# Performance work log

Hardware: AMD Instinct MI355X
Metric: run time of the kernel (lower is better)

## Reference

```python
import jax, jax.numpy as jnp
import numpy as np

N = 4096
DEG = 16.0
KC = 64  # max closed-neighborhood size supported (deg~16 graph => safe)


def setup_inputs() -> dict:
    key = jax.random.key(0)
    ks = jax.random.split(key, 6)
    u = jax.random.uniform(ks[0], (N, N))
    upper = jnp.triu((u < (DEG / N)).astype(jnp.float32), k=1)
    adj = upper + upper.T  # symmetric 0/1, zero diagonal
    d = 64
    return {
        'adj': adj,
        'e_w': jax.random.normal(ks[1], (15, d), dtype=jnp.float32) * 0.25,
        'e_b': jnp.zeros((d,), jnp.float32),
        'w1': jax.random.normal(ks[2], (3, d, d), dtype=jnp.float32) * 0.125,
        'b1': jnp.zeros((3, d), jnp.float32),
        'w2': jax.random.normal(ks[3], (3, d, d), dtype=jnp.float32) * 0.125,
        'b2': jnp.zeros((3, d), jnp.float32),
        'eps': jnp.zeros((3,), jnp.float32),
    }


def cr_feat(adj):
    n = adj.shape[0]
    m = adj + jnp.eye(n, dtype=adj.dtype)  # closed-neighborhood indicator rows [N,N]
    k = m.sum(1)                            # |S_v|
    D = m @ adj                             # D[v,u] = degree of u inside S_v (A symmetric)
    E = 0.5 * jnp.sum(m * D, axis=1)        # edges inside S_v
    W = jnp.sum(m * D * (D - 1.0) * 0.5, axis=1)  # wedges inside S_v
    vals, idx = jax.lax.top_k(m, KC)        # members of S_v (padded)
    valid = (vals > 0.5).astype(adj.dtype)
    sub = adj[idx[:, :, None], idx[:, None, :]]        # [N,KC,KC] induced subgraph
    sub = sub * valid[:, :, None] * valid[:, None, :]
    T = jnp.einsum('vij,vjk,vki->v', sub, sub, sub) / 6.0  # triangles inside S_v
    f3 = T
    f2 = W - 3.0 * T
    f1 = E * (k - 2.0) - 2.0 * f2 - 3.0 * f3
    tot = k * (k - 1.0) * (k - 2.0) / 6.0   # C(k,3) = total triples
    f0 = tot - f1 - f2 - f3
    f = jnp.stack([f0, f1, f2, f3], axis=1)
    f = jnp.where((k >= 3.0)[:, None], f, 0.0)  # original skips |nb|<3
    return f / (jnp.sum(f, axis=1, keepdims=True) + 1e-10)


def ww_feat(adj):
    a2 = adj @ adj
    a4 = a2 @ a2                             # matrix_power(adj, 4)
    vals, _ = jax.lax.top_k(a4, 8)           # per-row sort desc, top 8
    return vals


def degree_feat(adj):
    d = adj.sum(1)
    diag_a2 = jnp.einsum('vu,uv->v', adj, adj)  # diag(A@A)
    return jnp.stack([d, d ** 2, diag_a2], axis=1)


def _forward(adj, e_w, e_b, w1, b1, w2, b2, eps):
    feats = jnp.concatenate([cr_feat(adj), ww_feat(adj), degree_feat(adj)], axis=1)  # [N,15]
    x = feats @ e_w + e_b
    for i in range(3):
        h = (1.0 + eps[i]) * x + adj @ x
        x = jax.nn.relu(h @ w1[i] + b1[i]) @ w2[i] + b2[i]
    return x.sum(0)


def reference(adj, e_w, e_b, w1, b1, w2, b2, eps):
    return _forward(adj, e_w, e_b, w1, b1, w2, b2, eps)
```

## Files before the change

kernel.cpp:

```cpp
#include <hip/hip_runtime.h>
#include <hip/hip_bf16.h>
#include <stdint.h>

#define NN 4096
#define MAXNZ 1536


__global__ __launch_bounds__(256) void scan_k(const float* __restrict__ adj,
                                              int* __restrict__ nbr,
                                              int* __restrict__ deg,
                                              unsigned long long* __restrict__ abits,
                                              float* __restrict__ feats) {
    __shared__ int nlist[4][64];
    int tid = threadIdx.x;
    int wv = tid >> 6, ln = tid & 63;
    int v = blockIdx.x * 4 + wv;
    size_t rb = (size_t)v * NN;
    int total = 0;
    unsigned long long w0 = 0;
    for (int base = 0; base < NN; base += 256) {
        float v0 = adj[rb + base + ln];
        float v1 = adj[rb + base + 64 + ln];
        float v2 = adj[rb + base + 128 + ln];
        float v3 = adj[rb + base + 192 + ln];
        int q4 = (base >> 8) << 2;
        {
            unsigned long long m = __ballot(v0 > 0.5f);
            if (v0 > 0.5f) {
                int pos = total + __popcll(m & ((1ull << ln) - 1ull));
                if (pos < 64) nlist[wv][pos] = base + ln;
            }
            if (ln == q4 + 0) w0 = m;
            total += __popcll(m);
        }
        {
            unsigned long long m = __ballot(v1 > 0.5f);
            if (v1 > 0.5f) {
                int pos = total + __popcll(m & ((1ull << ln) - 1ull));
                if (pos < 64) nlist[wv][pos] = base + 64 + ln;
            }
            if (ln == q4 + 1) w0 = m;
            total += __popcll(m);
        }
        {
            unsigned long long m = __ballot(v2 > 0.5f);
            if (v2 > 0.5f) {
                int pos = total + __popcll(m & ((1ull << ln) - 1ull));
                if (pos < 64) nlist[wv][pos] = base + 128 + ln;
            }
            if (ln == q4 + 2) w0 = m;
            total += __popcll(m);
        }
        {
            unsigned long long m = __ballot(v3 > 0.5f);
            if (v3 > 0.5f) {
                int pos = total + __popcll(m & ((1ull << ln) - 1ull));
                if (pos < 64) nlist[wv][pos] = base + 192 + ln;
            }
            if (ln == q4 + 3) w0 = m;
            total += __popcll(m);
        }
    }
    abits[(size_t)v * 64 + ln] = w0;
    int degL = min(total, 64);
    if (ln < degL) nbr[v * 64 + ln] = nlist[wv][ln];
    if (ln == 0) {
        deg[v] = total;
        float degf = (float)total;
        feats[v * 16 + 12] = degf;
        feats[v * 16 + 13] = degf * degf;
        feats[v * 16 + 14] = degf;
    }
}

__global__ __launch_bounds__(256) void cra2_k(const unsigned long long* __restrict__ abits,
                                              const int* __restrict__ nbr,
                                              const int* __restrict__ deg,
                                              unsigned int* __restrict__ csr,
                                              int* __restrict__ cnt,
                                              unsigned char* __restrict__ ncb,
                                              float* __restrict__ feats) {
    __shared__ __align__(16) unsigned int smem[NN + 136];
    int tid = threadIdx.x;
    int bid = blockIdx.x;
    int wv = tid >> 6, ln = tid & 63;

    if (bid < NN) {
        unsigned int* acc   = smem;
        int* us             = (int*)(smem + NN);
        int* dus            = (int*)(smem + NN + 64);
        unsigned int* wsumS = smem + NN + 128;
        int v = bid;
        {
            uint4 z = {0u, 0u, 0u, 0u};
            #pragma unroll
            for (int i = 0; i < 4; i++) ((uint4*)acc)[tid + 256 * i] = z;
        }
        int dv = min(deg[v], 64);
        if (tid < dv) {
            int u = nbr[v * 64 + tid];
            us[tid] = u;
            dus[tid] = min(deg[u], 64);
        }
        __syncthreads();
        for (int p = tid; p < dv * 64; p += 256) {
            int i = p >> 6, wi = p & 63;
            int u = us[i];
            if (wi < dus[i]) atomicAdd(&acc[nbr[u * 64 + wi]], 1u);
        }
        __syncthreads();
        unsigned int local = 0;
        #pragma unroll
        for (int m = 0; m < 16; m++) {
            unsigned int a = acc[tid + 256 * m];
            local += (a + 14u) / 15u;
        }
        unsigned int incl = local;
        #pragma unroll
        for (int off = 1; off < 64; off <<= 1) {
            unsigned int n = (unsigned int)__shfl_up((int)incl, off, 64);
            if (ln >= off) incl += n;
        }
        if (ln == 63) wsumS[wv] = incl;
        __syncthreads();
        unsigned int wprefix = 0, tot = 0;
        #pragma unroll
        for (int q = 0; q < 4; q++) {
            unsigned int s = wsumS[q];
            if (q < wv) wprefix += s;
            tot += s;
        }
        unsigned int pos = wprefix + (incl - local);
        unsigned short* dst = (unsigned short*)((char*)csr + (size_t)v * 3072);
        #pragma unroll
        for (int m = 0; m < 16; m++) {
            unsigned int a = acc[tid + 256 * m];
            unsigned int col = (unsigned int)(tid + 256 * m);
            while (a) {
                unsigned int w = a > 15u ? 15u : a;
                if (pos < 1520u) dst[pos] = (unsigned short)((w << 12) | col);
                pos++;
                a -= w;
            }
        }
        unsigned int bs = min(tot, 1520u);
        unsigned int padto = (bs + 7u) & ~7u;
        if (tid < padto - bs) dst[bs + tid] = (unsigned short)(bs + tid);
        if (tid == 0) {
            cnt[v] = (int)bs;
            ncb[v] = (unsigned char)(padto >> 3);
        }
    } else {
        unsigned long long* rows = (unsigned long long*)smem;
        int* mems = (int*)(smem + 1024);
        int v = (bid - NN) * 4 + wv;

        int dv = deg[v];
        int degL = min(dv, 64);
        int c = min(dv + 1, 64);

        int nl = (ln < degL) ? nbr[v * 64 + ln] : 0;
        int isless = (ln < degL && nl < v) ? 1 : 0;
        int pos = isless;
        #pragma unroll
        for (int off = 32; off; off >>= 1) pos += __shfl_xor(pos, off, 64);

        int mem = 0;
        if (ln < c) {
            if (ln < pos)       mem = nl;
            else if (ln == pos) mem = v;
            else                mem = nbr[v * 64 + ln - 1];
        }
        mems[wv * 64 + ln] = mem;
        __syncthreads();

        unsigned long long mask = 0ull;
        {
            const unsigned long long* rowb = abits + (size_t)mem * 64;
            for (int j = 0; j < c; j++) {
                int mj = mems[wv * 64 + j];
                unsigned long long w = rowb[mj >> 6];
                mask |= ((w >> (mj & 63)) & 1ull) << j;
            }
        }
        if (ln >= c) mask = 0ull;
        rows[wv * 64 + ln] = mask;
        __syncthreads();

        int tpart = 0;
        float epart = 0.f, wpart = 0.f;
        if (ln < c) {
            unsigned long long mm = mask;
            while (mm) {
                int j = __ffsll(mm) - 1;
                mm &= mm - 1;
                tpart += __popcll(mask & rows[wv * 64 + j]);
            }
            if (ln != pos) {
                int cn = __popcll(rows[wv * 64 + pos] & mask);
                float D = (float)cn + 1.0f;
                epart = D;
                wpart = D * (D - 1.0f) * 0.5f;
            }
        }
        float es = epart, wsum2 = wpart;
        int ts = tpart;
        #pragma unroll
        for (int off = 32; off; off >>= 1) {
            es += __shfl_xor(es, off, 64);
            wsum2 += __shfl_xor(wsum2, off, 64);
            ts += __shfl_xor(ts, off, 64);
        }

        if (ln == 0) {
            float degf = (float)dv;
            float k = degf + 1.0f;
            float E = 0.5f * (es + degf);
            float W = wsum2 + degf * (degf - 1.0f) * 0.5f;
            float T = (float)ts / 6.0f;
            float f3 = T;
            float f2 = W - 3.0f * T;
            float f1 = E * (k - 2.0f) - 2.0f * f2 - 3.0f * f3;
            float tot2 = k * (k - 1.0f) * (k - 2.0f) / 6.0f;
            float f0 = tot2 - f1 - f2 - f3;
            if (k < 3.0f) { f0 = f1 = f2 = f3 = 0.f; }
            float s = f0 + f1 + f2 + f3 + 1e-10f;
            feats[v * 16 + 0] = f0 / s;
            feats[v * 16 + 1] = f1 / s;
            feats[v * 16 + 2] = f2 / s;
            feats[v * 16 + 3] = f3 / s;
        }
    }
}

__global__ __launch_bounds__(1024) void order_k(const unsigned char* __restrict__ ncb,
                                                int* __restrict__ ord) {
    __shared__ unsigned int bcnt[192];
    __shared__ unsigned int bbase[192];
    int tid = threadIdx.x;
    if (tid < 192) bcnt[tid] = 0u;
    __syncthreads();
    unsigned char myk[4];
    #pragma unroll
    for (int j = 0; j < 4; j++) {
        int v = tid * 4 + j;
        myk[j] = ncb[v];
        atomicAdd(&bcnt[myk[j]], 1u);
    }
    __syncthreads();
    if (tid == 0) {
        unsigned int run = 0;
        for (int b = 191; b >= 0; b--) { bbase[b] = run; run += bcnt[b]; }
    }
    __syncthreads();
    #pragma unroll
    for (int j = 0; j < 4; j++) {
        int v = tid * 4 + j;
        unsigned int p = atomicAdd(&bbase[myk[j]], 1u);
        ord[p] = v;
    }
}

__device__ __forceinline__ void do8(unsigned int* acc, uint4 E, unsigned int W) {
    atomicAdd(&acc[E.x & 0xFFFu],         W * ((E.x >> 12) & 0xFu));
    atomicAdd(&acc[(E.x >> 16) & 0xFFFu], W * (E.x >> 28));
    atomicAdd(&acc[E.y & 0xFFFu],         W * ((E.y >> 12) & 0xFu));
    atomicAdd(&acc[(E.y >> 16) & 0xFFFu], W * (E.y >> 28));
    atomicAdd(&acc[E.z & 0xFFFu],         W * ((E.z >> 12) & 0xFu));
    atomicAdd(&acc[(E.z >> 16) & 0xFFFu], W * (E.z >> 28));
    atomicAdd(&acc[E.w & 0xFFFu],         W * ((E.w >> 12) & 0xFu));
    atomicAdd(&acc[(E.w >> 16) & 0xFFFu], W * (E.w >> 28));
}

__global__ __launch_bounds__(512) void a4row_k(const unsigned int* __restrict__ csr,
                                               const int* __restrict__ cnt,
                                               const unsigned char* __restrict__ ncb,
                                               const int* __restrict__ ord,
                                               const float* __restrict__ feats,
                                               const float* __restrict__ e_w,
                                               const float* __restrict__ e_b,
                                               float* __restrict__ x0) {
    __shared__ unsigned int acc[NN];
    __shared__ __align__(16) unsigned int rowe[MAXNZ];
    __shared__ unsigned int wtops[64];
    int tid = threadIdx.x;
    int wv = tid >> 6, ln = tid & 63;
    int v = ord[blockIdx.x];

    {
        uint4 z = {0u, 0u, 0u, 0u};
        #pragma unroll
        for (int i = 0; i < 2; i++) ((uint4*)acc)[tid + 512 * i] = z;
    }

    int nv = cnt[v];
    int nvp = (nv + 7) & ~7;
    const unsigned short* rowv = (const unsigned short*)((const char*)csr + (size_t)v * 3072);
    for (int i = tid; i < nvp; i += 512) {
        unsigned int e = rowv[i];
        unsigned int u = e & 0xFFFu;
        unsigned int w = e >> 12;
        unsigned int nc = w ? (unsigned int)ncb[u] : 0u;
        rowe[i] = u | (w << 12) | (nc << 16);
    }
    __syncthreads();

    const uint4* csr4 = (const uint4*)csr;
    for (int i0 = wv * 4; i0 < nvp; i0 += 32) {
        uint4 q = *(const uint4*)&rowe[i0];
        int c1 = (int)(q.x >> 16);
        int c2 = c1 + (int)(q.y >> 16);
        int c3 = c2 + (int)(q.z >> 16);
        int tot = c3 + (int)(q.w >> 16);
        unsigned int s0 = ((q.x & 0xFFFu) * 192u + 1024u)                    | (((q.x >> 12) & 0xFu) << 21);
        unsigned int s1 = ((q.y & 0xFFFu) * 192u + 1024u - (unsigned int)c1) | (((q.y >> 12) & 0xFu) << 21);
        unsigned int s2 = ((q.z & 0xFFFu) * 192u + 1024u - (unsigned int)c2) | (((q.z >> 12) & 0xFu) << 21);
        unsigned int s3 = ((q.w & 0xFFFu) * 192u + 1024u - (unsigned int)c3) | (((q.w >> 12) & 0xFu) << 21);
        for (int g = ln; g < tot; g += 64) {
            unsigned int sel = (g < c1) ? s0 : ((g < c2) ? s1 : ((g < c3) ? s2 : s3));
            unsigned int idx = (sel & 0x1FFFFFu) + (unsigned int)g - 1024u;
            uint4 E = csr4[idx];
            do8(acc, E, sel >> 21);
        }
    }
    __syncthreads();

    unsigned int best[8];
    #pragma unroll
    for (int q = 0; q < 8; q++) best[q] = 0u;
    #pragma unroll
    for (int m = 0; m < 8; m++) {
        unsigned int val = acc[tid + 512 * m];
        if (val > best[7]) {
            best[7] = val;
            #pragma unroll
            for (int s = 7; s > 0; s--) {
                if (best[s] > best[s - 1]) {
                    unsigned int t2 = best[s - 1]; best[s - 1] = best[s]; best[s] = t2;
                } else break;
            }
        }
    }

    unsigned int wave_val = 0u;
    #pragma unroll
    for (int r = 0; r < 8; r++) {
        unsigned int m = best[0];
        #pragma unroll
        for (int off = 32; off; off >>= 1)
            m = max(m, (unsigned int)__shfl_xor((int)m, off, 64));
        unsigned long long bb = __ballot(best[0] == m);
        int src = __ffsll(bb) - 1;
        if (ln == src) {
            #pragma unroll
            for (int s = 0; s < 7; s++) best[s] = best[s + 1];
            best[7] = 0u;
        }
        if (ln == r) wave_val = m;
    }
    if (ln < 8) wtops[wv * 8 + ln] = wave_val;
    __syncthreads();

    if (wv == 0) {
        unsigned int cand = wtops[ln];
        unsigned int myv = 0u;
        #pragma unroll
        for (int r = 0; r < 8; r++) {
            unsigned int m = cand;
            #pragma unroll
            for (int off = 32; off; off >>= 1)
                m = max(m, (unsigned int)__shfl_xor((int)m, off, 64));
            unsigned long long bb = __ballot(cand == m);
            int src = __ffsll(bb) - 1;
            if (ln == src) cand = 0u;
            if (ln == r) myv = m;
        }
        int d = ln;
        float s = e_b[d];
        s += feats[v * 16 + 0]  * e_w[0 * 64 + d];
        s += feats[v * 16 + 1]  * e_w[1 * 64 + d];
        s += feats[v * 16 + 2]  * e_w[2 * 64 + d];
        s += feats[v * 16 + 3]  * e_w[3 * 64 + d];
        #pragma unroll
        for (int j = 0; j < 8; j++) {
            float mj = (float)(unsigned int)__shfl((int)myv, j, 64);
            s += mj * e_w[(4 + j) * 64 + d];
        }
        s += feats[v * 16 + 12] * e_w[12 * 64 + d];
        s += feats[v * 16 + 13] * e_w[13 * 64 + d];
        s += feats[v * 16 + 14] * e_w[14 * 64 + d];
        x0[(size_t)v * 64 + d] = s;
    }
}

__global__ __launch_bounds__(256) void layer_k(const float* __restrict__ xin,
                                               float* __restrict__ xout,
                                               const float* __restrict__ w1,
                                               const float* __restrict__ b1,
                                               const float* __restrict__ w2,
                                               const float* __restrict__ b2,
                                               const float* __restrict__ eps,
                                               const int* __restrict__ nbr,
                                               const int* __restrict__ deg,
                                               float* __restrict__ out,
                                               int li) {
    __shared__ float wL[4096];
    __shared__ float h[4][64], t[4][64];
    int tid = threadIdx.x;
    int wv = tid >> 6, d = tid & 63;
    int v = blockIdx.x * 4 + wv;

    {
        const float4* src = (const float4*)(w1 + li * 4096);
        #pragma unroll
        for (int i = 0; i < 4; i++) ((float4*)wL)[tid + 256 * i] = src[tid + 256 * i];
    }

    float xv = xin[(size_t)v * 64 + d];
    int dv = min(deg[v], 64);
    const int* nl = nbr + v * 64;
    float agg = 0.f;
    int j = 0;
    for (; j + 4 <= dv; j += 4) {
        int n0 = nl[j], n1 = nl[j + 1], n2 = nl[j + 2], n3 = nl[j + 3];
        float a0 = xin[(size_t)n0 * 64 + d];
        float a1 = xin[(size_t)n1 * 64 + d];
        float a2v = xin[(size_t)n2 * 64 + d];
        float a3 = xin[(size_t)n3 * 64 + d];
        agg += (a0 + a1) + (a2v + a3);
    }
    for (; j < dv; j++) agg += xin[(size_t)nl[j] * 64 + d];
    float hv = (1.0f + eps[li]) * xv + agg;
    h[wv][d] = hv;
    __syncthreads();

    float s = b1[li * 64 + d];
    #pragma unroll 8
    for (int k = 0; k < 64; k++) s += h[wv][k] * wL[k * 64 + d];
    s = fmaxf(s, 0.f);
    t[wv][d] = s;
    __syncthreads();

    {
        const float4* src = (const float4*)(w2 + li * 4096);
        #pragma unroll
        for (int i = 0; i < 4; i++) ((float4*)wL)[tid + 256 * i] = src[tid + 256 * i];
    }
    __syncthreads();

    float o = b2[li * 64 + d];
    #pragma unroll 8
    for (int k = 0; k < 64; k++) o += t[wv][k] * wL[k * 64 + d];
    if (li == 2) {
        h[wv][d] = o;
        __syncthreads();
        if (wv == 0)
            atomicAdd(&out[d], (h[0][d] + h[1][d]) + (h[2][d] + h[3][d]));
    } else {
        xout[(size_t)v * 64 + d] = o;
    }
}

extern "C" void kernel_launch(void* const* d_in, const int* in_sizes, int n_in,
                              void* d_out, int out_size, void* d_ws, size_t ws_size,
                              hipStream_t stream) {
    const float* adj = (const float*)d_in[0];
    const float* e_w = (const float*)d_in[1];
    const float* e_b = (const float*)d_in[2];
    const float* w1  = (const float*)d_in[3];
    const float* b1  = (const float*)d_in[4];
    const float* w2  = (const float*)d_in[5];
    const float* b2  = (const float*)d_in[6];
    const float* eps = (const float*)d_in[7];
    float* out = (float*)d_out;

    char* ws = (char*)d_ws;
    unsigned int*       csr     = (unsigned int*)(ws);
    int*                nbr     = (int*)(ws + 25165824);
    int*                deg     = (int*)(ws + 26214400);
    int*                cnt     = (int*)(ws + 26230784);
    float*              feats   = (float*)(ws + 26247168);
    float*              x0      = (float*)(ws + 26509312);
    float*              x1      = (float*)(ws + 27557888);
    unsigned long long* abits   = (unsigned long long*)(ws + 28868608);
    unsigned char*      ncb     = (unsigned char*)(ws + 30965760);
    int*                ord     = (int*)(ws + 30969856);

    hipMemsetAsync(out, 0, 64 * sizeof(float), stream);
    scan_k<<<1024, 256, 0, stream>>>(adj, nbr, deg, abits, feats);
    cra2_k<<<5120, 256, 0, stream>>>(abits, nbr, deg, csr, cnt, ncb, feats);
    order_k<<<1, 1024, 0, stream>>>(ncb, ord);
    a4row_k<<<4096, 512, 0, stream>>>(csr, cnt, ncb, ord, feats, e_w, e_b, x0);
    layer_k<<<1024, 256, 0, stream>>>(x0, x1, w1, b1, w2, b2, eps, nbr, deg, out, 0);
    layer_k<<<1024, 256, 0, stream>>>(x1, x0, w1, b1, w2, b2, eps, nbr, deg, out, 1);
    layer_k<<<1024, 256, 0, stream>>>(x0, x1, w1, b1, w2, b2, eps, nbr, deg, out, 2);
}
```

Baseline: 278.1 us.

## Vectorize adjacency scan with float4 and interleave CSR storage layout

```diff
diff --git a/kernel.cpp b/kernel.cpp
--- a/kernel.cpp
+++ b/kernel.cpp
@@ -18,46 +18,19 @@
     size_t rb = (size_t)v * NN;
     int total = 0;
     unsigned long long w0 = 0;
+    const float4* row4 = (const float4*)(adj + rb);
     for (int base = 0; base < NN; base += 256) {
-        float v0 = adj[rb + base + ln];
-        float v1 = adj[rb + base + 64 + ln];
-        float v2 = adj[rb + base + 128 + ln];
-        float v3 = adj[rb + base + 192 + ln];
+        float4 f = row4[(base >> 2) + ln];
         int q4 = (base >> 8) << 2;
-        {
-            unsigned long long m = __ballot(v0 > 0.5f);
-            if (v0 > 0.5f) {
+        #pragma unroll
+        for (int j = 0; j < 4; j++) {
+            float vj = (j == 0) ? f.x : (j == 1) ? f.y : (j == 2) ? f.z : f.w;
+            unsigned long long m = __ballot(vj > 0.5f);
+            if (vj > 0.5f) {
                 int pos = total + __popcll(m & ((1ull << ln) - 1ull));
-                if (pos < 64) nlist[wv][pos] = base + ln;
-            }
-            if (ln == q4 + 0) w0 = m;
-            total += __popcll(m);
-        }
-        {
-            unsigned long long m = __ballot(v1 > 0.5f);
-            if (v1 > 0.5f) {
-                int pos = total + __popcll(m & ((1ull << ln) - 1ull));
-                if (pos < 64) nlist[wv][pos] = base + 64 + ln;
-            }
-            if (ln == q4 + 1) w0 = m;
-            total += __popcll(m);
-        }
-        {
-            unsigned long long m = __ballot(v2 > 0.5f);
-            if (v2 > 0.5f) {
-                int pos = total + __popcll(m & ((1ull << ln) - 1ull));
-                if (pos < 64) nlist[wv][pos] = base + 128 + ln;
-            }
-            if (ln == q4 + 2) w0 = m;
-            total += __popcll(m);
-        }
-        {
-            unsigned long long m = __ballot(v3 > 0.5f);
-            if (v3 > 0.5f) {
-                int pos = total + __popcll(m & ((1ull << ln) - 1ull));
-                if (pos < 64) nlist[wv][pos] = base + 192 + ln;
-            }
-            if (ln == q4 + 3) w0 = m;
+                if (pos < 64) nlist[wv][pos] = base + 4 * ln + j;
+            }
+            if (ln == q4 + j) w0 = m;
             total += __popcll(m);
         }
     }
@@ -131,6 +104,10 @@
             tot += s;
         }
         unsigned int pos = wprefix + (incl - local);
+        unsigned int bs = min(tot, 1520u);
+        unsigned int padto = (bs + 7u) & ~7u;
+        unsigned int D = padto >> 3;
+        unsigned long long M = (unsigned long long)(0xFFFFFFFFu / max(D, 1u)) + 1ull;
         unsigned short* dst = (unsigned short*)((char*)csr + (size_t)v * 3072);
         #pragma unroll
         for (int m = 0; m < 16; m++) {
@@ -138,14 +115,21 @@
             unsigned int col = (unsigned int)(tid + 256 * m);
             while (a) {
                 unsigned int w = a > 15u ? 15u : a;
-                if (pos < 1520u) dst[pos] = (unsigned short)((w << 12) | col);
+                if (pos < 1520u) {
+                    unsigned int q = (unsigned int)(((unsigned long long)pos * M) >> 32);
+                    unsigned int r = pos - q * D;
+                    dst[8u * r + q] = (unsigned short)((w << 12) | col);
+                }
                 pos++;
                 a -= w;
             }
         }
-        unsigned int bs = min(tot, 1520u);
-        unsigned int padto = (bs + 7u) & ~7u;
-        if (tid < padto - bs) dst[bs + tid] = (unsigned short)(bs + tid);
+        if (tid < padto - bs) {
+            unsigned int p = bs + tid;
+            unsigned int q = (unsigned int)(((unsigned long long)p * M) >> 32);
+            unsigned int r = p - q * D;
+            dst[8u * r + q] = (unsigned short)(p & 0xFFFu);
+        }
         if (tid == 0) {
             cnt[v] = (int)bs;
             ncb[v] = (unsigned char)(padto >> 3);
@@ -179,8 +163,8 @@
             const unsigned long long* rowb = abits + (size_t)mem * 64;
             for (int j = 0; j < c; j++) {
                 int mj = mems[wv * 64 + j];
-                unsigned long long w = rowb[mj >> 6];
-                mask |= ((w >> (mj & 63)) & 1ull) << j;
+                unsigned long long w = rowb[((mj >> 8) << 2) | (mj & 3)];
+                mask |= ((w >> ((mj >> 2) & 63)) & 1ull) << j;
             }
         }
         if (ln >= c) mask = 0ull;
@@ -198,9 +182,9 @@
             }
             if (ln != pos) {
                 int cn = __popcll(rows[wv * 64 + pos] & mask);
-                float D = (float)cn + 1.0f;
-                epart = D;
-                wpart = D * (D - 1.0f) * 0.5f;
+                float D2 = (float)cn + 1.0f;
+                epart = D2;
+                wpart = D2 * (D2 - 1.0f) * 0.5f;
             }
         }
         float es = epart, wsum2 = wpart;
```

Result: slower. 291.3 us (+4.8%).
